# Kernel tuning notes

Hardware: AMD Instinct MI355X
Metric: run time of the kernel (lower is better)

The kernel has to match this reference:

```python
import jax, jax.numpy as jnp
import numpy as np

N_OUT = 4096
N_IN = 4096
N_SPARSE = 1024  # int(0.25 * N_IN)
BATCH, SEQ = 4, 2048


def setup_inputs() -> dict:
    key = jax.random.key(0)
    k1, k2, k3 = jax.random.split(key, 3)
    x = jax.random.normal(k1, (BATCH, SEQ, N_IN), dtype=jnp.float32)
    sparse_values = jax.random.normal(k2, (N_OUT, N_SPARSE), dtype=jnp.float32)
    # static equivalent of the boolean sparse_mask: sorted unique column indices
    sparse_idx = jnp.sort(jax.random.permutation(k3, N_IN)[:N_SPARSE]).astype(jnp.int64)
    return {"x": x, "sparse_values": sparse_values, "sparse_idx": sparse_idx}


def reference(x, sparse_values, sparse_idx):
    # x[..., mask] @ sparse_values.T  ->  gather columns then GEMM
    x_g = jnp.take(x, sparse_idx, axis=-1)          # [B, S, n_sparse]
    return jnp.einsum('bsk,ok->bso', x_g, sparse_values)  # [B, S, n_out]
```

## Files before the change

### kernel.cpp

```cpp
#include <hip/hip_runtime.h>
#include <hip/hip_bf16.h>

#define NOUT  4096
#define KDIM  1024
#define MROWS 8192

typedef __attribute__((ext_vector_type(8))) short bf16x8;
typedef __attribute__((ext_vector_type(16))) float f32x16;

__device__ __forceinline__ unsigned short f2bf(float f) {
  union { float f; unsigned int u; } c; c.f = f;
  unsigned int lsb = (c.u >> 16) & 1u;
  c.u += 0x7fffu + lsb;
  return (unsigned short)(c.u >> 16);
}

__device__ __forceinline__ void gload_lds16(const void* g, void* l) {
  __builtin_amdgcn_global_load_lds(
      (const __attribute__((address_space(1))) void*)g,
      (__attribute__((address_space(3))) void*)l, 16, 0, 0);
}

#define FENCE() asm volatile("" ::: "memory")
#define BAR() do { FENCE(); __builtin_amdgcn_s_barrier(); FENCE(); } while (0)
#define VMW(n) asm volatile("s_waitcnt vmcnt(" #n ")" ::: "memory")

__global__ __launch_bounds__(512) void prep(const float* __restrict__ x,
                                            const void* __restrict__ idx_raw,
                                            const float* __restrict__ w,
                                            unsigned short* __restrict__ xg,
                                            unsigned short* __restrict__ wb) {
  __shared__ float rows[16384];
  __shared__ int sidx[1024];
  const int b = blockIdx.x;
  const int t = threadIdx.x;

  if (b < 2048) {
    const long long* p64 = (const long long*)idx_raw;
    const int* p32 = (const int*)idx_raw;
    const bool is64 = ((unsigned long long)p64[0]) < 4096ull;
    const float* src = x + (size_t)b * 4 * 4096;
#pragma unroll
    for (int i = 0; i < 8; ++i)
      ((float4*)rows)[t + 512 * i] = ((const float4*)src)[t + 512 * i];
    if (is64) {
      sidx[t] = (int)p64[t];
      sidx[t + 512] = (int)p64[t + 512];
    } else {
      sidx[t] = p32[t];
      sidx[t + 512] = p32[t + 512];
    }
    __syncthreads();
    ushort4* dst = (ushort4*)(xg + (size_t)b * 4 * 1024);
#pragma unroll
    for (int i = 0; i < 2; ++i) {
      const int q = t + 512 * i;
      const int e = 4 * q;
      const int rbase = (e >> 10) * 4096;
      const int k = e & 1023;
      ushort4 o;
      o.x = f2bf(rows[rbase + sidx[k + 0]]);
      o.y = f2bf(rows[rbase + sidx[k + 1]]);
      o.z = f2bf(rows[rbase + sidx[k + 2]]);
      o.w = f2bf(rows[rbase + sidx[k + 3]]);
      dst[q] = o;
    }
  } else {
    const int i0 = (b - 2048) * 2048 + t;
#pragma unroll
    for (int j = 0; j < 4; ++j) {
      float4 v = ((const float4*)w)[i0 + 512 * j];
      ushort4 o;
      o.x = f2bf(v.x); o.y = f2bf(v.y); o.z = f2bf(v.z); o.w = f2bf(v.w);
      ((ushort4*)wb)[i0 + 512 * j] = o;
    }
  }
}

__global__ __launch_bounds__(512, 2) void gemm256(const unsigned short* __restrict__ A,
                                                  const unsigned short* __restrict__ B,
                                                  float* __restrict__ C) {
  __shared__ __align__(16) unsigned short lds[65536];

  const int tid = threadIdx.x;
  const int lane = tid & 63;
  const int wid = tid >> 6;
  const int wm = wid >> 2, wn = wid & 3;
  const int l31 = lane & 31, lh = lane >> 5;
  const int sw = l31 & 7;

  const int bn0 = blockIdx.x * 256;
  const int bm0 = blockIdx.y * 256;

  const int pr = tid >> 3;
  const int cg = (tid & 7) ^ (pr & 7);
  const unsigned short* Ag = A + (size_t)(bm0 + pr) * KDIM + cg * 8;
  const unsigned short* Bg = B + (size_t)(bn0 + pr) * KDIM + cg * 8;
  const int tid8 = tid * 8;

  const int cK0 = ((0 + lh) ^ sw) * 8;
  const int cK1 = ((2 + lh) ^ sw) * 8;
  const int cK2 = ((4 + lh) ^ sw) * 8;
  const int cK3 = ((6 + lh) ^ sw) * 8;
  const int aRow = wm * 8192 + l31 * 64;
  const int bRow = 32768 + wn * 4096 + l31 * 64;

  f32x16 acc[4][2] = {};
  bf16x8 a[2][4], bN0[4], bN1[4];

#define LOAD_A(D, MH) do {                                                        \
    const unsigned short* _p = lds + (D) * 16384 + aRow + (MH) * 4096;            \
    a[0][0] = *(const bf16x8*)(_p + cK0);        a[0][1] = *(const bf16x8*)(_p + cK1);         \
    a[0][2] = *(const bf16x8*)(_p + cK2);        a[0][3] = *(const bf16x8*)(_p + cK3);         \
    a[1][0] = *(const bf16x8*)(_p + 2048 + cK0); a[1][1] = *(const bf16x8*)(_p + 2048 + cK1);  \
    a[1][2] = *(const bf16x8*)(_p + 2048 + cK2); a[1][3] = *(const bf16x8*)(_p + 2048 + cK3);  \
  } while (0)

#define LOAD_B(D, NF, R) do {                                                     \
    const unsigned short* _p = lds + (D) * 16384 + bRow + (NF) * 2048;            \
    R[0] = *(const bf16x8*)(_p + cK0); R[1] = *(const bf16x8*)(_p + cK1);         \
    R[2] = *(const bf16x8*)(_p + cK2); R[3] = *(const bf16x8*)(_p + cK3);         \
  } while (0)

#define STAGE_A(D, T, H) do {                                                     \
    gload_lds16(Ag + (size_t)((H) * 128) * KDIM + (T) * 64,                       \
                lds + (D) * 16384 + (H) * 8192 + tid8);                           \
    gload_lds16(Ag + (size_t)((H) * 128 + 64) * KDIM + (T) * 64,                  \
                lds + (D) * 16384 + (H) * 8192 + 4096 + tid8);                    \
  } while (0)

#define STAGE_B(D, T, H) do {                                                     \
    gload_lds16(Bg + (size_t)((H) * 128) * KDIM + (T) * 64,                       \
                lds + 32768 + (D) * 16384 + (H) * 8192 + tid8);                   \
    gload_lds16(Bg + (size_t)((H) * 128 + 64) * KDIM + (T) * 64,                  \
                lds + 32768 + (D) * 16384 + (H) * 8192 + 4096 + tid8);            \
  } while (0)

#define MFMA_Q(MH, NH, R) do {                                                    \
    __builtin_amdgcn_s_setprio(1);                                                \
    _Pragma("unroll") for (int kb = 0; kb < 4; ++kb) {                            \
      _Pragma("unroll") for (int mf = 0; mf < 2; ++mf) {                          \
        acc[(MH)*2+mf][NH] = __builtin_amdgcn_mfma_f32_32x32x16_bf16(             \
            a[mf][kb], R[kb], acc[(MH)*2+mf][NH], 0, 0, 0);                       \
      }                                                                           \
    }                                                                             \
    __builtin_amdgcn_s_setprio(0);                                                \
  } while (0)

  STAGE_B(0, 0, 0); STAGE_B(0, 0, 1);
  STAGE_A(0, 0, 0); STAGE_A(0, 0, 1);
  STAGE_B(1, 1, 0); STAGE_B(1, 1, 1);
  VMW(4);
  BAR();

  for (int i = 0; i < 8; ++i) {
    const int tA1 = 2 * i + 1;
    const int tN0 = (2 * i + 2) & 15;
    const int tN1 = (2 * i + 3) & 15;

    LOAD_A(0, 0); LOAD_B(0, 0, bN0); STAGE_A(1, tA1, 0);
    BAR(); MFMA_Q(0, 0, bN0); BAR();
    LOAD_B(0, 1, bN1); STAGE_A(1, tA1, 1);
    BAR(); MFMA_Q(0, 1, bN1); BAR();
    LOAD_A(0, 1); STAGE_B(0, tN0, 0);
    BAR(); MFMA_Q(1, 0, bN0); BAR();
    STAGE_B(0, tN0, 1);
    BAR(); MFMA_Q(1, 1, bN1); VMW(4); BAR();
    LOAD_A(1, 0); LOAD_B(1, 0, bN0); STAGE_A(0, tN0, 0);
    BAR(); MFMA_Q(0, 0, bN0); BAR();
    LOAD_B(1, 1, bN1); STAGE_A(0, tN0, 1);
    BAR(); MFMA_Q(0, 1, bN1); BAR();
    LOAD_A(1, 1); STAGE_B(1, tN1, 0);
    BAR(); MFMA_Q(1, 0, bN0); BAR();
    STAGE_B(1, tN1, 1);
    BAR(); MFMA_Q(1, 1, bN1); VMW(4); BAR();
  }

  VMW(0);
  float* base = C + (size_t)(bm0 + wm * 128) * NOUT + bn0 + wn * 64;
#pragma unroll
  for (int mf = 0; mf < 4; ++mf)
#pragma unroll
    for (int nf = 0; nf < 2; ++nf) {
      f32x16 v = acc[mf][nf];
#pragma unroll
      for (int r = 0; r < 16; ++r) {
        const int rowi = mf * 32 + (r & 3) + 8 * (r >> 2) + 4 * lh;
        base[(size_t)rowi * NOUT + nf * 32 + l31] = v[r];
      }
    }

#undef LOAD_A
#undef LOAD_B
#undef STAGE_A
#undef STAGE_B
#undef MFMA_Q
}

extern "C" void kernel_launch(void* const* d_in, const int* in_sizes, int n_in,
                              void* d_out, int out_size, void* d_ws, size_t ws_size,
                              hipStream_t stream) {
  const float* x   = (const float*)d_in[0];
  const float* sv  = (const float*)d_in[1];
  const void*  idx = d_in[2];
  float* out = (float*)d_out;

  unsigned short* xg = (unsigned short*)d_ws;
  unsigned short* wb = xg + (size_t)MROWS * KDIM;

  prep<<<2560, 512, 0, stream>>>(x, idx, sv, xg, wb);

  dim3 grid(NOUT / 256, MROWS / 256);
  gemm256<<<grid, 512, 0, stream>>>(xg, wb, out);
}
```

Baseline: 119.2 us.

## Gather directly from global in prep and strengthen LDS XOR swizzle in GEMM

The prep kernel no longer stages four full fp32 rows and the index table in shared memory. Each thread now reads its four indices with vector loads and gathers the x values straight from global memory, which removes the 64KB LDS footprint and a block barrier but turns the gather into scattered global reads. The GEMM's LDS swizzle also folds row bits 3-4 into the XOR on both the staging and read side, aiming to cut LDS bank conflicts in the MFMA operand loads.

```diff
diff --git a/kernel.cpp b/kernel.cpp
--- a/kernel.cpp
+++ b/kernel.cpp
@@ -30,39 +30,32 @@
                                             const float* __restrict__ w,
                                             unsigned short* __restrict__ xg,
                                             unsigned short* __restrict__ wb) {
-  __shared__ float rows[16384];
-  __shared__ int sidx[1024];
   const int b = blockIdx.x;
   const int t = threadIdx.x;
 
   if (b < 2048) {
     const long long* p64 = (const long long*)idx_raw;
-    const int* p32 = (const int*)idx_raw;
     const bool is64 = ((unsigned long long)p64[0]) < 4096ull;
-    const float* src = x + (size_t)b * 4 * 4096;
-#pragma unroll
-    for (int i = 0; i < 8; ++i)
-      ((float4*)rows)[t + 512 * i] = ((const float4*)src)[t + 512 * i];
-    if (is64) {
-      sidx[t] = (int)p64[t];
-      sidx[t + 512] = (int)p64[t + 512];
-    } else {
-      sidx[t] = p32[t];
-      sidx[t + 512] = p32[t + 512];
-    }
-    __syncthreads();
+    const float* xb = x + (size_t)b * 4 * 4096;
     ushort4* dst = (ushort4*)(xg + (size_t)b * 4 * 1024);
 #pragma unroll
     for (int i = 0; i < 2; ++i) {
       const int q = t + 512 * i;
-      const int e = 4 * q;
-      const int rbase = (e >> 10) * 4096;
-      const int k = e & 1023;
+      const int row = q >> 8;
+      const int k = (q & 255) * 4;
+      int ka0, ka1, ka2, ka3;
+      if (is64) {
+        longlong2 v0 = ((const longlong2*)p64)[(k >> 1) + 0];
+        longlong2 v1 = ((const longlong2*)p64)[(k >> 1) + 1];
+        ka0 = (int)v0.x; ka1 = (int)v0.y; ka2 = (int)v1.x; ka3 = (int)v1.y;
+      } else {
+        int4 v = ((const int4*)idx_raw)[k >> 2];
+        ka0 = v.x; ka1 = v.y; ka2 = v.z; ka3 = v.w;
+      }
+      const float* rp = xb + row * 4096;
       ushort4 o;
-      o.x = f2bf(rows[rbase + sidx[k + 0]]);
-      o.y = f2bf(rows[rbase + sidx[k + 1]]);
-      o.z = f2bf(rows[rbase + sidx[k + 2]]);
-      o.w = f2bf(rows[rbase + sidx[k + 3]]);
+      o.x = f2bf(rp[ka0]); o.y = f2bf(rp[ka1]);
+      o.z = f2bf(rp[ka2]); o.w = f2bf(rp[ka3]);
       dst[q] = o;
     }
   } else {
@@ -87,21 +80,21 @@
   const int wid = tid >> 6;
   const int wm = wid >> 2, wn = wid & 3;
   const int l31 = lane & 31, lh = lane >> 5;
-  const int sw = l31 & 7;
 
   const int bn0 = blockIdx.x * 256;
   const int bm0 = blockIdx.y * 256;
 
   const int pr = tid >> 3;
-  const int cg = (tid & 7) ^ (pr & 7);
+  const int cg = (tid & 7) ^ (pr & 7) ^ ((pr >> 3) & 3);
   const unsigned short* Ag = A + (size_t)(bm0 + pr) * KDIM + cg * 8;
   const unsigned short* Bg = B + (size_t)(bn0 + pr) * KDIM + cg * 8;
   const int tid8 = tid * 8;
 
-  const int cK0 = ((0 + lh) ^ sw) * 8;
-  const int cK1 = ((2 + lh) ^ sw) * 8;
-  const int cK2 = ((4 + lh) ^ sw) * 8;
-  const int cK3 = ((6 + lh) ^ sw) * 8;
+  const int sw8 = (l31 & 7) ^ (l31 >> 3);
+  const int cK0 = (lh ^ sw8) * 8;
+  const int cK1 = cK0 ^ 16;
+  const int cK2 = cK0 ^ 32;
+  const int cK3 = cK0 ^ 48;
   const int aRow = wm * 8192 + l31 * 64;
   const int bRow = 32768 + wn * 4096 + l31 * 64;
 
```

Result: faster. 114.6 us (-3.9%).

## Peel last K iteration, interleave epilogue stores with MFMAs, strengthen LDS swizzle

Applied to the files above, without the earlier changes.

Changes the LDS XOR swizzle to also mix in row-group bits, aiming to cut bank conflicts on the fragment reads. Peels the final main-loop iteration so no wasted wrap-around loads are staged. It then overlaps the last tile's MFMAs with per-quadrant output stores. The peeled tail drops most barriers, which relies on correct waitcnt placement.

```diff
diff --git a/kernel.cpp b/kernel.cpp
--- a/kernel.cpp
+++ b/kernel.cpp
@@ -24,6 +24,7 @@
 #define FENCE() asm volatile("" ::: "memory")
 #define BAR() do { FENCE(); __builtin_amdgcn_s_barrier(); FENCE(); } while (0)
 #define VMW(n) asm volatile("s_waitcnt vmcnt(" #n ")" ::: "memory")
+#define LGKM0() asm volatile("s_waitcnt lgkmcnt(0)" ::: "memory")
 
 __global__ __launch_bounds__(512) void prep(const float* __restrict__ x,
                                             const void* __restrict__ idx_raw,
@@ -87,21 +88,21 @@
   const int wid = tid >> 6;
   const int wm = wid >> 2, wn = wid & 3;
   const int l31 = lane & 31, lh = lane >> 5;
-  const int sw = l31 & 7;
 
   const int bn0 = blockIdx.x * 256;
   const int bm0 = blockIdx.y * 256;
 
   const int pr = tid >> 3;
-  const int cg = (tid & 7) ^ (pr & 7);
+  const int cg = (tid & 7) ^ (pr & 7) ^ ((pr >> 3) & 3);
   const unsigned short* Ag = A + (size_t)(bm0 + pr) * KDIM + cg * 8;
   const unsigned short* Bg = B + (size_t)(bn0 + pr) * KDIM + cg * 8;
   const int tid8 = tid * 8;
 
-  const int cK0 = ((0 + lh) ^ sw) * 8;
-  const int cK1 = ((2 + lh) ^ sw) * 8;
-  const int cK2 = ((4 + lh) ^ sw) * 8;
-  const int cK3 = ((6 + lh) ^ sw) * 8;
+  const int sw8 = (l31 & 7) ^ (l31 >> 3);
+  const int cK0 = (lh ^ sw8) * 8;
+  const int cK1 = cK0 ^ 16;
+  const int cK2 = cK0 ^ 32;
+  const int cK3 = cK0 ^ 48;
   const int aRow = wm * 8192 + l31 * 64;
   const int bRow = 32768 + wn * 4096 + l31 * 64;
 
@@ -153,10 +154,10 @@
   VMW(4);
   BAR();
 
-  for (int i = 0; i < 8; ++i) {
+  for (int i = 0; i < 7; ++i) {
     const int tA1 = 2 * i + 1;
-    const int tN0 = (2 * i + 2) & 15;
-    const int tN1 = (2 * i + 3) & 15;
+    const int tN0 = 2 * i + 2;
+    const int tN1 = 2 * i + 3;
 
     LOAD_A(0, 0); LOAD_B(0, 0, bN0); STAGE_A(1, tA1, 0);
     BAR(); MFMA_Q(0, 0, bN0); BAR();
@@ -176,25 +177,37 @@
     BAR(); MFMA_Q(1, 1, bN1); VMW(4); BAR();
   }
 
-  VMW(0);
+  STAGE_A(1, 15, 0); STAGE_A(1, 15, 1);
+
+  LOAD_A(0, 0); LOAD_B(0, 0, bN0); MFMA_Q(0, 0, bN0);
+  LOAD_B(0, 1, bN1);               MFMA_Q(0, 1, bN1);
+  LOAD_A(0, 1);                    MFMA_Q(1, 0, bN0);
+                                   MFMA_Q(1, 1, bN1);
+
+  VMW(0); LGKM0(); BAR();
+
   float* base = C + (size_t)(bm0 + wm * 128) * NOUT + bn0 + wn * 64;
-#pragma unroll
-  for (int mf = 0; mf < 4; ++mf)
-#pragma unroll
-    for (int nf = 0; nf < 2; ++nf) {
-      f32x16 v = acc[mf][nf];
-#pragma unroll
-      for (int r = 0; r < 16; ++r) {
-        const int rowi = mf * 32 + (r & 3) + 8 * (r >> 2) + 4 * lh;
-        base[(size_t)rowi * NOUT + nf * 32 + l31] = v[r];
-      }
-    }
+#define STORE_Q(MH, NH) do {                                                      \
+    _Pragma("unroll") for (int mf = 0; mf < 2; ++mf) {                            \
+      f32x16 v = acc[(MH)*2+mf][NH];                                              \
+      _Pragma("unroll") for (int r = 0; r < 16; ++r) {                            \
+        const int rowi = ((MH)*2+mf) * 32 + (r & 3) + 8 * (r >> 2) + 4 * lh;      \
+        base[(size_t)rowi * NOUT + (NH) * 32 + l31] = v[r];                       \
+      }                                                                           \
+    }                                                                             \
+  } while (0)
+
+  LOAD_A(1, 0); LOAD_B(1, 0, bN0); MFMA_Q(0, 0, bN0); STORE_Q(0, 0);
+  LOAD_B(1, 1, bN1);               MFMA_Q(0, 1, bN1); STORE_Q(0, 1);
+  LOAD_A(1, 1);                    MFMA_Q(1, 0, bN0); STORE_Q(1, 0);
+                                   MFMA_Q(1, 1, bN1); STORE_Q(1, 1);
 
 #undef LOAD_A
 #undef LOAD_B
 #undef STAGE_A
 #undef STAGE_B
 #undef MFMA_Q
+#undef STORE_Q
 }
 
 extern "C" void kernel_launch(void* const* d_in, const int* in_sizes, int n_in,
```

Result: faster. 113.6 us (-4.7%).
